# Kernel tuning notes

Hardware: AMD Instinct MI355X
Metric: run time of the kernel (lower is better)

## Reference

```python
import jax, jax.numpy as jnp
import numpy as np

NUM_GROUPS = 8
K = 2


def setup_inputs() -> dict:
    key = jax.random.key(0)
    k1, k2, k3 = jax.random.split(key, 3)
    b, l, d = 4, 4096, 2048
    g, k = NUM_GROUPS, K
    hdg = d // g  # 256
    x = jax.random.normal(k1, (b, l, d), dtype=jnp.float32)
    Wg = jax.random.normal(k2, (d, g), dtype=jnp.float32) * 0.02  # gate (no bias)
    Wm = jax.random.normal(k3, (k * hdg, k * hdg), dtype=jnp.float32) * 0.02  # inner Linear
    bm = jnp.zeros((k * hdg,), dtype=jnp.float32)
    return {"x": x, "Wg": Wg, "Wm": Wm, "bm": bm}


def reference(x, Wg, Wm, bm):
    b, l, d = x.shape
    g, k = NUM_GROUPS, K
    hdg = d // g
    # gate: softmax + topk over groups
    S = jax.nn.softmax(x @ Wg, axis=-1)            # [b, l, g]
    G, I = jax.lax.top_k(S, k)                     # [b, l, k] each
    x4 = x.reshape(b, l, g, hdg)
    # gather selected feature groups
    sel = jnp.take_along_axis(x4, I[..., None], axis=2)  # [b, l, k, hdg]
    h = (G[..., None] * sel).reshape(b, l, k * hdg)
    # inner model (Linear)
    h = h @ Wm + bm
    h = h.reshape(b, l, k, hdg)
    # scatter back into original groups
    bi = jnp.arange(b)[:, None, None]
    li = jnp.arange(l)[None, :, None]
    out = x4.at[bi, li, I].set(h)
    return out.reshape(b, l, d)
```

## Files before the change

kernel.cpp:

```cpp
#include <hip/hip_runtime.h>
#include <hip/hip_bf16.h>

#define NTOK   16384
#define DIM    2048
#define NGRP   8
#define HDG    256
#define NIN    512

typedef float f32x4 __attribute__((ext_vector_type(4)));
typedef short bf16x8 __attribute__((ext_vector_type(8)));

static __device__ __forceinline__ unsigned short f2bf(float f) {
    unsigned int u = __builtin_bit_cast(unsigned int, f);
    u = (u + 0x7fffu + ((u >> 16) & 1u)) >> 16;
    return (unsigned short)u;
}

__global__ __launch_bounds__(256) void prep_wm(const float* __restrict__ Wm,
                                               ushort* __restrict__ WmT) {
    __shared__ float tile[64][65];
    const int bk = blockIdx.x * 64;
    const int bn = blockIdx.y * 64;
    const int t = threadIdx.x;
    const int r = t >> 4;
    const int c = (t & 15) * 4;
#pragma unroll
    for (int i = 0; i < 4; i++) {
        const float4 v = *(const float4*)&Wm[(bk + r + i * 16) * 512 + bn + c];
        tile[r + i * 16][c + 0] = v.x;
        tile[r + i * 16][c + 1] = v.y;
        tile[r + i * 16][c + 2] = v.z;
        tile[r + i * 16][c + 3] = v.w;
    }
    __syncthreads();
#pragma unroll
    for (int i = 0; i < 4; i++) {
        const int n = r + i * 16;
        ushort4 o;
        o.x = f2bf(tile[c + 0][n]);
        o.y = f2bf(tile[c + 1][n]);
        o.z = f2bf(tile[c + 2][n]);
        o.w = f2bf(tile[c + 3][n]);
        *(ushort4*)&WmT[(bn + n) * 512 + bk + c] = o;
    }
}

__global__ __launch_bounds__(256) void gate_gather(
        const float* __restrict__ x, const float* __restrict__ Wg,
        float* __restrict__ out, ushort* __restrict__ hbuf,
        int* __restrict__ Isel) {
    const int t = threadIdx.x;
    const int jg = t >> 5;
    float wgr[8][8];
#pragma unroll
    for (int j = 0; j < 8; j++) {
        const float4 a = *(const float4*)&Wg[(t * 8 + j) * 8];
        const float4 b = *(const float4*)&Wg[(t * 8 + j) * 8 + 4];
        wgr[j][0] = a.x; wgr[j][1] = a.y; wgr[j][2] = a.z; wgr[j][3] = a.w;
        wgr[j][4] = b.x; wgr[j][5] = b.y; wgr[j][6] = b.z; wgr[j][7] = b.w;
    }
    __shared__ float red[4][8];
    const int tok0 = blockIdx.x * 8;
    for (int tt = 0; tt < 8; tt++) {
        const int tok = tok0 + tt;
        const float4 x0 = *(const float4*)&x[tok * DIM + t * 8];
        const float4 x1 = *(const float4*)&x[tok * DIM + t * 8 + 4];
        const float xr[8] = {x0.x, x0.y, x0.z, x0.w, x1.x, x1.y, x1.z, x1.w};
        float acc[8];
#pragma unroll
        for (int g = 0; g < 8; g++) acc[g] = 0.f;
#pragma unroll
        for (int j = 0; j < 8; j++)
#pragma unroll
            for (int g = 0; g < 8; g++)
                acc[g] = fmaf(xr[j], wgr[j][g], acc[g]);
#pragma unroll
        for (int g = 0; g < 8; g++) {
            float v = acc[g];
            v += __shfl_xor(v, 1, 64);
            v += __shfl_xor(v, 2, 64);
            v += __shfl_xor(v, 4, 64);
            v += __shfl_xor(v, 8, 64);
            v += __shfl_xor(v, 16, 64);
            v += __shfl_xor(v, 32, 64);
            acc[g] = v;
        }
        __syncthreads();
        if ((t & 63) == 0) {
#pragma unroll
            for (int g = 0; g < 8; g++) red[t >> 6][g] = acc[g];
        }
        __syncthreads();
        float lg[8];
#pragma unroll
        for (int g = 0; g < 8; g++)
            lg[g] = red[0][g] + red[1][g] + red[2][g] + red[3][g];
        float m = lg[0];
#pragma unroll
        for (int g = 1; g < 8; g++) m = fmaxf(m, lg[g]);
        float sum = 0.f;
#pragma unroll
        for (int g = 0; g < 8; g++) sum += __expf(lg[g] - m);
        int i0 = 0; float b0 = lg[0];
#pragma unroll
        for (int g = 1; g < 8; g++) { if (lg[g] > b0) { b0 = lg[g]; i0 = g; } }
        int i1 = -1; float b1 = -3.4e38f;
#pragma unroll
        for (int g = 0; g < 8; g++) { if (g != i0 && lg[g] > b1) { b1 = lg[g]; i1 = g; } }
        const float inv = 1.0f / sum;
        const float G0 = __expf(b0 - m) * inv;
        const float G1 = __expf(b1 - m) * inv;

        if (jg == i0 || jg == i1) {
            const float gv  = (jg == i0) ? G0 : G1;
            const int  slot = (jg == i0) ? 0 : 1;
            int4 pk;
            pk.x = (int)f2bf(gv * xr[0]) | ((int)f2bf(gv * xr[1]) << 16);
            pk.y = (int)f2bf(gv * xr[2]) | ((int)f2bf(gv * xr[3]) << 16);
            pk.z = (int)f2bf(gv * xr[4]) | ((int)f2bf(gv * xr[5]) << 16);
            pk.w = (int)f2bf(gv * xr[6]) | ((int)f2bf(gv * xr[7]) << 16);
            *(int4*)&hbuf[tok * NIN + slot * HDG + (t & 31) * 8] = pk;
        } else {
            *(float4*)&out[tok * DIM + t * 8]     = x0;
            *(float4*)&out[tok * DIM + t * 8 + 4] = x1;
        }
        if (t == 0) { Isel[tok * 2] = i0; Isel[tok * 2 + 1] = i1; }
    }
}

__global__ __launch_bounds__(256) void gemm_scatter(
        const ushort* __restrict__ h, const ushort* __restrict__ WmT,
        const float* __restrict__ bm, const int* __restrict__ Isel,
        float* __restrict__ out) {
    __shared__ ushort As[128][40];
    __shared__ ushort Bs[128][40];
    const int t = threadIdx.x;
    const int lane = t & 63;
    const int wave = t >> 6;
    const int wr = (wave >> 1) * 64;
    const int wc = (wave & 1) * 64;
    const int row0 = blockIdx.x * 128;
    const int n0 = blockIdx.y * 128;

    const int sr = t >> 2;
    const int sc = (t & 3) * 8;

    f32x4 acc[4][4];
#pragma unroll
    for (int i = 0; i < 4; i++)
#pragma unroll
        for (int j = 0; j < 4; j++)
            acc[i][j] = (f32x4){0.f, 0.f, 0.f, 0.f};

    for (int kk = 0; kk < 512; kk += 32) {
        __syncthreads();
        *(int4*)&As[sr][sc]      = *(const int4*)&h[(row0 + sr) * 512 + kk + sc];
        *(int4*)&As[sr + 64][sc] = *(const int4*)&h[(row0 + sr + 64) * 512 + kk + sc];
        *(int4*)&Bs[sr][sc]      = *(const int4*)&WmT[(n0 + sr) * 512 + kk + sc];
        *(int4*)&Bs[sr + 64][sc] = *(const int4*)&WmT[(n0 + sr + 64) * 512 + kk + sc];
        __syncthreads();
        const int fr = lane & 15;
        const int kh = (lane >> 4) * 8;
        bf16x8 av[4], bv[4];
#pragma unroll
        for (int i = 0; i < 4; i++) {
            av[i] = *(const bf16x8*)&As[wr + i * 16 + fr][kh];
            bv[i] = *(const bf16x8*)&Bs[wc + i * 16 + fr][kh];
        }
#pragma unroll
        for (int i = 0; i < 4; i++)
#pragma unroll
            for (int j = 0; j < 4; j++)
                acc[i][j] = __builtin_amdgcn_mfma_f32_16x16x32_bf16(
                    av[i], bv[j], acc[i][j], 0, 0, 0);
    }

    const int fr = lane & 15;
    const int rq = (lane >> 4) * 4;
    const int s    = (n0 + wc) >> 8;
    const int ninh = (n0 + wc) & 255;
    float bmv[4];
#pragma unroll
    for (int j = 0; j < 4; j++) bmv[j] = bm[n0 + wc + j * 16 + fr];
#pragma unroll
    for (int i = 0; i < 4; i++) {
#pragma unroll
        for (int r = 0; r < 4; r++) {
            const int row = row0 + wr + i * 16 + rq + r;
            const int grp = Isel[row * 2 + s];
            float* op = &out[row * DIM + grp * HDG + ninh];
#pragma unroll
            for (int j = 0; j < 4; j++)
                op[j * 16 + fr] = acc[i][j][r] + bmv[j];
        }
    }
}

extern "C" void kernel_launch(void* const* d_in, const int* in_sizes, int n_in,
                              void* d_out, int out_size, void* d_ws, size_t ws_size,
                              hipStream_t stream) {
    const float* x  = (const float*)d_in[0];
    const float* Wg = (const float*)d_in[1];
    const float* Wm = (const float*)d_in[2];
    const float* bm = (const float*)d_in[3];
    float* out = (float*)d_out;

    char* ws = (char*)d_ws;
    ushort* hbuf = (ushort*)ws;
    ushort* WmT  = (ushort*)(ws + (size_t)16 * 1024 * 1024);
    int*    Isel = (int*)(ws + (size_t)16 * 1024 * 1024 + 512 * 1024);

    prep_wm<<<dim3(8, 8), 256, 0, stream>>>(Wm, WmT);
    gate_gather<<<NTOK / 8, 256, 0, stream>>>(x, Wg, out, hbuf, Isel);
    gemm_scatter<<<dim3(NTOK / 128, NIN / 128), 256, 0, stream>>>(hbuf, WmT, bm, Isel, out);
}
```

Before: 276.3 us.

## Restructure gate reduction, double-buffer GEMM loads, transpose GEMM for vector stores

The gate kernel now reduces all eight group logits with a butterfly exchange that halves shuffle count, and it does the per-token block syncs once per 8 tokens instead of twice per token. It also re-reads x to gather per token, with each half-wave handling one token. The GEMM kernel double-buffers LDS with register prefetch, dropping one barrier per k-step. It swaps operand roles so accumulators hold contiguous output columns, allowing float4 scatter stores, and reorders the grid so N-blocks sharing a token tile run adjacent. The cost is a second read of x in the gate kernel (likely cache-hit) and more registers.

```diff
diff --git a/kernel.cpp b/kernel.cpp
--- a/kernel.cpp
+++ b/kernel.cpp
@@ -50,7 +50,8 @@
         float* __restrict__ out, ushort* __restrict__ hbuf,
         int* __restrict__ Isel) {
     const int t = threadIdx.x;
-    const int jg = t >> 5;
+    const int lane = t & 63;
+    const int wave = t >> 6;
     float wgr[8][8];
 #pragma unroll
     for (int j = 0; j < 8; j++) {
@@ -59,8 +60,14 @@
         wgr[j][0] = a.x; wgr[j][1] = a.y; wgr[j][2] = a.z; wgr[j][3] = a.w;
         wgr[j][4] = b.x; wgr[j][5] = b.y; wgr[j][6] = b.z; wgr[j][7] = b.w;
     }
-    __shared__ float red[4][8];
+    __shared__ float red[8][4][8];
     const int tok0 = blockIdx.x * 8;
+
+    const bool b0 = lane & 1;
+    const bool b1 = lane & 2;
+    const bool b2 = lane & 4;
+
+#pragma unroll
     for (int tt = 0; tt < 8; tt++) {
         const int tok = tok0 + tt;
         const float4 x0 = *(const float4*)&x[tok * DIM + t * 8];
@@ -74,57 +81,94 @@
 #pragma unroll
             for (int g = 0; g < 8; g++)
                 acc[g] = fmaf(xr[j], wgr[j][g], acc[g]);
-#pragma unroll
-        for (int g = 0; g < 8; g++) {
-            float v = acc[g];
-            v += __shfl_xor(v, 1, 64);
-            v += __shfl_xor(v, 2, 64);
-            v += __shfl_xor(v, 4, 64);
-            v += __shfl_xor(v, 8, 64);
-            v += __shfl_xor(v, 16, 64);
-            v += __shfl_xor(v, 32, 64);
-            acc[g] = v;
-        }
-        __syncthreads();
-        if ((t & 63) == 0) {
-#pragma unroll
-            for (int g = 0; g < 8; g++) red[t >> 6][g] = acc[g];
-        }
-        __syncthreads();
-        float lg[8];
-#pragma unroll
-        for (int g = 0; g < 8; g++)
-            lg[g] = red[0][g] + red[1][g] + red[2][g] + red[3][g];
-        float m = lg[0];
-#pragma unroll
-        for (int g = 1; g < 8; g++) m = fmaxf(m, lg[g]);
-        float sum = 0.f;
-#pragma unroll
-        for (int g = 0; g < 8; g++) sum += __expf(lg[g] - m);
-        int i0 = 0; float b0 = lg[0];
-#pragma unroll
-        for (int g = 1; g < 8; g++) { if (lg[g] > b0) { b0 = lg[g]; i0 = g; } }
-        int i1 = -1; float b1 = -3.4e38f;
-#pragma unroll
-        for (int g = 0; g < 8; g++) { if (g != i0 && lg[g] > b1) { b1 = lg[g]; i1 = g; } }
-        const float inv = 1.0f / sum;
-        const float G0 = __expf(b0 - m) * inv;
-        const float G1 = __expf(b1 - m) * inv;
-
-        if (jg == i0 || jg == i1) {
-            const float gv  = (jg == i0) ? G0 : G1;
-            const int  slot = (jg == i0) ? 0 : 1;
+        float n_[4];
+#pragma unroll
+        for (int j = 0; j < 4; j++) {
+            const float keep = b0 ? acc[2 * j + 1] : acc[2 * j];
+            const float send = b0 ? acc[2 * j] : acc[2 * j + 1];
+            n_[j] = keep + __shfl_xor(send, 1, 64);
+        }
+        float m_[2];
+#pragma unroll
+        for (int j = 0; j < 2; j++) {
+            const float keep = b1 ? n_[2 * j + 1] : n_[2 * j];
+            const float send = b1 ? n_[2 * j] : n_[2 * j + 1];
+            m_[j] = keep + __shfl_xor(send, 2, 64);
+        }
+        float v;
+        {
+            const float keep = b2 ? m_[1] : m_[0];
+            const float send = b2 ? m_[0] : m_[1];
+            v = keep + __shfl_xor(send, 4, 64);
+        }
+        v += __shfl_xor(v, 8, 64);
+        v += __shfl_xor(v, 16, 64);
+        v += __shfl_xor(v, 32, 64);
+        if (lane < 8) red[tt][wave][lane] = v;
+    }
+    __syncthreads();
+
+    const int ll = lane & 31;
+    const int tok_local = wave * 2 + (lane >> 5);
+    const int tok = tok0 + tok_local;
+
+    float v = red[tok_local][ll >> 3][ll & 7];
+    v += __shfl_xor(v, 8, 64);
+    v += __shfl_xor(v, 16, 64);
+    float c[8];
+    c[0] = v;
+    c[1] = __shfl_xor(c[0], 1, 64);
+    c[2] = __shfl_xor(c[0], 2, 64);
+    c[3] = __shfl_xor(c[1], 2, 64);
+    c[4] = __shfl_xor(c[0], 4, 64);
+    c[5] = __shfl_xor(c[1], 4, 64);
+    c[6] = __shfl_xor(c[2], 4, 64);
+    c[7] = __shfl_xor(c[3], 4, 64);
+    const int gbase = ll & 7;
+
+    float m = c[0];
+#pragma unroll
+    for (int j = 1; j < 8; j++) m = fmaxf(m, c[j]);
+    float sum = 0.f;
+#pragma unroll
+    for (int j = 0; j < 8; j++) sum += __expf(c[j] - m);
+    int i0 = 8; float v0 = -3.4e38f;
+#pragma unroll
+    for (int j = 0; j < 8; j++) {
+        const int g = gbase ^ j;
+        if (c[j] > v0 || (c[j] == v0 && g < i0)) { v0 = c[j]; i0 = g; }
+    }
+    int i1 = 8; float v1 = -3.4e38f;
+#pragma unroll
+    for (int j = 0; j < 8; j++) {
+        const int g = gbase ^ j;
+        if (g != i0 && (c[j] > v1 || (c[j] == v1 && g < i1))) { v1 = c[j]; i1 = g; }
+    }
+    const float inv = 1.0f / sum;
+    const float G0 = __expf(v0 - m) * inv;
+    const float G1 = __expf(v1 - m) * inv;
+
+#pragma unroll
+    for (int cgrp = 0; cgrp < 8; cgrp++) {
+        const float4 f0 = *(const float4*)&x[tok * DIM + cgrp * HDG + ll * 8];
+        const float4 f1 = *(const float4*)&x[tok * DIM + cgrp * HDG + ll * 8 + 4];
+        if (cgrp == i0 || cgrp == i1) {
+            const float gv  = (cgrp == i0) ? G0 : G1;
+            const int slot  = (cgrp == i0) ? 0 : 1;
             int4 pk;
-            pk.x = (int)f2bf(gv * xr[0]) | ((int)f2bf(gv * xr[1]) << 16);
-            pk.y = (int)f2bf(gv * xr[2]) | ((int)f2bf(gv * xr[3]) << 16);
-            pk.z = (int)f2bf(gv * xr[4]) | ((int)f2bf(gv * xr[5]) << 16);
-            pk.w = (int)f2bf(gv * xr[6]) | ((int)f2bf(gv * xr[7]) << 16);
-            *(int4*)&hbuf[tok * NIN + slot * HDG + (t & 31) * 8] = pk;
+            pk.x = (int)f2bf(gv * f0.x) | ((int)f2bf(gv * f0.y) << 16);
+            pk.y = (int)f2bf(gv * f0.z) | ((int)f2bf(gv * f0.w) << 16);
+            pk.z = (int)f2bf(gv * f1.x) | ((int)f2bf(gv * f1.y) << 16);
+            pk.w = (int)f2bf(gv * f1.z) | ((int)f2bf(gv * f1.w) << 16);
+            *(int4*)&hbuf[tok * NIN + slot * HDG + ll * 8] = pk;
         } else {
-            *(float4*)&out[tok * DIM + t * 8]     = x0;
-            *(float4*)&out[tok * DIM + t * 8 + 4] = x1;
-        }
-        if (t == 0) { Isel[tok * 2] = i0; Isel[tok * 2 + 1] = i1; }
+            *(float4*)&out[tok * DIM + cgrp * HDG + ll * 8]     = f0;
+            *(float4*)&out[tok * DIM + cgrp * HDG + ll * 8 + 4] = f1;
+        }
+    }
+    if (ll == 0) {
+        int2 s2; s2.x = i0; s2.y = i1;
+        *(int2*)&Isel[tok * 2] = s2;
     }
 }
 
@@ -132,19 +176,29 @@
         const ushort* __restrict__ h, const ushort* __restrict__ WmT,
         const float* __restrict__ bm, const int* __restrict__ Isel,
         float* __restrict__ out) {
-    __shared__ ushort As[128][40];
-    __shared__ ushort Bs[128][40];
+    __shared__ ushort Hs[2][128][40];
+    __shared__ ushort Ws[2][128][40];
     const int t = threadIdx.x;
     const int lane = t & 63;
     const int wave = t >> 6;
-    const int wr = (wave >> 1) * 64;
-    const int wc = (wave & 1) * 64;
-    const int row0 = blockIdx.x * 128;
-    const int n0 = blockIdx.y * 128;
+    const int wn = (wave >> 1) * 64;
+    const int wt = (wave & 1) * 64;
+    const int n_blk = blockIdx.x * 128;
+    const int tok_blk = blockIdx.y * 128;
 
     const int sr = t >> 2;
     const int sc = (t & 3) * 8;
 
+    const ushort* hp0 = &h[(tok_blk + sr) * 512 + sc];
+    const ushort* hp1 = hp0 + 64 * 512;
+    const ushort* wp0 = &WmT[(n_blk + sr) * 512 + sc];
+    const ushort* wp1 = wp0 + 64 * 512;
+
+    int4 rh0 = *(const int4*)hp0;
+    int4 rh1 = *(const int4*)hp1;
+    int4 rw0 = *(const int4*)wp0;
+    int4 rw1 = *(const int4*)wp1;
+
     f32x4 acc[4][4];
 #pragma unroll
     for (int i = 0; i < 4; i++)
@@ -152,21 +206,28 @@
         for (int j = 0; j < 4; j++)
             acc[i][j] = (f32x4){0.f, 0.f, 0.f, 0.f};
 
-    for (int kk = 0; kk < 512; kk += 32) {
+    const int fr = lane & 15;
+    const int kh = (lane >> 4) * 8;
+
+    for (int k = 0; k < 16; ++k) {
+        const int b = k & 1;
+        *(int4*)&Hs[b][sr][sc]      = rh0;
+        *(int4*)&Hs[b][sr + 64][sc] = rh1;
+        *(int4*)&Ws[b][sr][sc]      = rw0;
+        *(int4*)&Ws[b][sr + 64][sc] = rw1;
         __syncthreads();
-        *(int4*)&As[sr][sc]      = *(const int4*)&h[(row0 + sr) * 512 + kk + sc];
-        *(int4*)&As[sr + 64][sc] = *(const int4*)&h[(row0 + sr + 64) * 512 + kk + sc];
-        *(int4*)&Bs[sr][sc]      = *(const int4*)&WmT[(n0 + sr) * 512 + kk + sc];
-        *(int4*)&Bs[sr + 64][sc] = *(const int4*)&WmT[(n0 + sr + 64) * 512 + kk + sc];
-        __syncthreads();
-        const int fr = lane & 15;
-        const int kh = (lane >> 4) * 8;
+        if (k < 15) {
+            const int off = (k + 1) * 32;
+            rh0 = *(const int4*)(hp0 + off);
+            rh1 = *(const int4*)(hp1 + off);
+            rw0 = *(const int4*)(wp0 + off);
+            rw1 = *(const int4*)(wp1 + off);
+        }
         bf16x8 av[4], bv[4];
 #pragma unroll
-        for (int i = 0; i < 4; i++) {
-            av[i] = *(const bf16x8*)&As[wr + i * 16 + fr][kh];
-            bv[i] = *(const bf16x8*)&Bs[wc + i * 16 + fr][kh];
-        }
+        for (int i = 0; i < 4; i++) av[i] = *(const bf16x8*)&Ws[b][wn + i * 16 + fr][kh];
+#pragma unroll
+        for (int j = 0; j < 4; j++) bv[j] = *(const bf16x8*)&Hs[b][wt + j * 16 + fr][kh];
 #pragma unroll
         for (int i = 0; i < 4; i++)
 #pragma unroll
@@ -175,23 +236,27 @@
                     av[i], bv[j], acc[i][j], 0, 0, 0);
     }
 
-    const int fr = lane & 15;
     const int rq = (lane >> 4) * 4;
-    const int s    = (n0 + wc) >> 8;
-    const int ninh = (n0 + wc) & 255;
-    float bmv[4];
-#pragma unroll
-    for (int j = 0; j < 4; j++) bmv[j] = bm[n0 + wc + j * 16 + fr];
-#pragma unroll
-    for (int i = 0; i < 4; i++) {
-#pragma unroll
-        for (int r = 0; r < 4; r++) {
-            const int row = row0 + wr + i * 16 + rq + r;
-            const int grp = Isel[row * 2 + s];
-            float* op = &out[row * DIM + grp * HDG + ninh];
-#pragma unroll
-            for (int j = 0; j < 4; j++)
-                op[j * 16 + fr] = acc[i][j][r] + bmv[j];
+    const int n_base = n_blk + wn;
+    const int s = n_base >> 8;
+    const int n_off_base = (n_base & 255) + rq;
+    float4 bmv[4];
+#pragma unroll
+    for (int i = 0; i < 4; i++) bmv[i] = *(const float4*)&bm[n_base + i * 16 + rq];
+#pragma unroll
+    for (int j = 0; j < 4; j++) {
+        const int tok = tok_blk + wt + j * 16 + fr;
+        const int2 sel = *(const int2*)&Isel[tok * 2];
+        const int grp = s ? sel.y : sel.x;
+        float* op = &out[tok * DIM + grp * HDG + n_off_base];
+#pragma unroll
+        for (int i = 0; i < 4; i++) {
+            float4 o;
+            o.x = acc[i][j][0] + bmv[i].x;
+            o.y = acc[i][j][1] + bmv[i].y;
+            o.z = acc[i][j][2] + bmv[i].z;
+            o.w = acc[i][j][3] + bmv[i].w;
+            *(float4*)&op[i * 16] = o;
         }
     }
 }
@@ -212,5 +277,5 @@
 
     prep_wm<<<dim3(8, 8), 256, 0, stream>>>(Wm, WmT);
     gate_gather<<<NTOK / 8, 256, 0, stream>>>(x, Wg, out, hbuf, Isel);
-    gemm_scatter<<<dim3(NTOK / 128, NIN / 128), 256, 0, stream>>>(hbuf, WmT, bm, Isel, out);
-}
+    gemm_scatter<<<dim3(NIN / 128, NTOK / 128), 256, 0, stream>>>(hbuf, WmT, bm, Isel, out);
+}
```

Result: slower. 283.2 us (+2.5%).
